# Optimization experiments

Measured on AMD Instinct MI355X. Metric: run time of the kernel, lower is better.

The kernel has to match this reference:

```python
import jax, jax.numpy as jnp
import numpy as np

N_NODES = 50000
N_EDGES = 1_600_000
IN_DIM = 128
HID = 64


def gcn_conv(x, src, dst, w, W, b, n):
    # PyG GCNConv(normalize=True, add_self_loops=True):
    # add self loops with weight 1, sym-normalize, x@W (no bias in lin), scatter-add, +bias
    loop = jnp.arange(n)
    s = jnp.concatenate([src, loop])
    d = jnp.concatenate([dst, loop])
    ww = jnp.concatenate([w, jnp.ones((n,), w.dtype)])
    deg = jax.ops.segment_sum(ww, d, num_segments=n)                 # [n]
    dis = jnp.where(deg > 0, jax.lax.rsqrt(deg), 0.0)                # deg^{-1/2}, inf->0
    norm = dis[s] * ww * dis[d]                                      # [E+n]
    h = x @ W                                                        # [n, out]
    msg = h[s] * norm[:, None]                                       # gather + scale
    out = jax.ops.segment_sum(msg, d, num_segments=n)                # scatter-add at dst
    return out + b


def setup_inputs() -> dict:
    key = jax.random.key(0)
    ks = jax.random.split(key, 9)
    X = jax.random.normal(ks[0], (N_NODES, IN_DIM), dtype=jnp.float32)
    edge_index = jax.random.randint(ks[1], (2, N_EDGES), 0, N_NODES, dtype=jnp.int64)
    edge_weight = jax.random.uniform(ks[2], (N_EDGES,), dtype=jnp.float32)
    s1 = 1.0 / np.sqrt(IN_DIM)
    s2 = 1.0 / np.sqrt(HID)
    W1 = jax.random.uniform(ks[3], (IN_DIM, HID), jnp.float32, -s1, s1)
    b1 = jax.random.uniform(ks[4], (HID,), jnp.float32, -s1, s1)
    W2 = jax.random.uniform(ks[5], (HID, HID), jnp.float32, -s2, s2)
    b2 = jax.random.uniform(ks[6], (HID,), jnp.float32, -s2, s2)
    Wl = jax.random.uniform(ks[7], (HID, 1), jnp.float32, -s2, s2)
    bl = jax.random.uniform(ks[8], (1,), jnp.float32, -s2, s2)
    return {"X": X, "edge_index": edge_index, "edge_weight": edge_weight,
            "W1": W1, "b1": b1, "W2": W2, "b2": b2, "Wl": Wl, "bl": bl}


def reference(X, edge_index, edge_weight, W1, b1, W2, b2, Wl, bl):
    n = X.shape[0]
    src, dst = edge_index[0], edge_index[1]
    h = jax.nn.relu(gcn_conv(X, src, dst, edge_weight, W1, b1, n))
    # F.dropout(p=0.2) is identity in eval mode
    h = jax.nn.relu(gcn_conv(h, src, dst, edge_weight, W2, b2, n))
    return jax.nn.sigmoid(h @ Wl + bl).squeeze(1)   # [n]
```

## Files before the change

### kernel.cpp

```cpp
#include <hip/hip_runtime.h>

typedef float f32x2 __attribute__((ext_vector_type(2)));

#define A2B 512
#define A2T 512
#define STG 3200

__device__ __forceinline__ long ld_idx(const void* idx, long pos, int is64) {
  return is64 ? (long)((const long long*)idx)[pos]
              : (long)((const int*)idx)[pos];
}

__device__ __forceinline__ int detect_is64(const void* idx) {
  const unsigned long long* p = (const unsigned long long*)idx;
  unsigned long long v = p[threadIdx.x & 63];
  return (__ballot((v >> 32) != 0ull) == 0ull) ? 1 : 0;
}

__device__ __forceinline__ int swz_group(int bid, int GP) {
  int r = bid & 7, q = bid >> 3;
  int j = q / GP;
  int i = q - j * GP;
  return (r + 8 * j) * GP + i;
}

__device__ __forceinline__ uint4 pack16_fp8(const float* acc) {
  uint4 o;
  unsigned v;
  v = 0;
  v = __builtin_amdgcn_cvt_pk_fp8_f32(acc[0],  acc[1],  v, false);
  v = __builtin_amdgcn_cvt_pk_fp8_f32(acc[2],  acc[3],  v, true);
  o.x = v; v = 0;
  v = __builtin_amdgcn_cvt_pk_fp8_f32(acc[4],  acc[5],  v, false);
  v = __builtin_amdgcn_cvt_pk_fp8_f32(acc[6],  acc[7],  v, true);
  o.y = v; v = 0;
  v = __builtin_amdgcn_cvt_pk_fp8_f32(acc[8],  acc[9],  v, false);
  v = __builtin_amdgcn_cvt_pk_fp8_f32(acc[10], acc[11], v, true);
  o.z = v; v = 0;
  v = __builtin_amdgcn_cvt_pk_fp8_f32(acc[12], acc[13], v, false);
  v = __builtin_amdgcn_cvt_pk_fp8_f32(acc[14], acc[15], v, true);
  o.w = v;
  return o;
}

__global__ __launch_bounds__(256) void k_front(const void* __restrict__ idx,
                                               unsigned* __restrict__ histT,
                                               long E, int chunk, unsigned M) {
  __shared__ unsigned cnt[256];
  const int t = threadIdx.x;
  const int b = blockIdx.x;
  const int is64 = detect_is64(idx);
  cnt[t] = 0;
  __syncthreads();
  const long e0 = (long)b * chunk;
  long e1 = e0 + chunk; if (e1 > E) e1 = E;
  for (long e = e0 + t; e < e1; e += 256) {
    unsigned d = (unsigned)ld_idx(idx, E + e, is64);
    atomicAdd(&cnt[__umulhi(d, M)], 1u);
  }
  __syncthreads();
  histT[(size_t)t * A2B + b] = cnt[t];
}

__global__ __launch_bounds__(256) void k_colscan(const unsigned* __restrict__ histT,
                                                 unsigned* __restrict__ baseT,
                                                 unsigned* __restrict__ colsum) {
  __shared__ unsigned sh[256];
  const int k = blockIdx.x, t = threadIdx.x;
  const uint2 v = ((const uint2*)(histT + (size_t)k * A2B))[t];
  unsigned s = v.x + v.y;
  sh[t] = s;
  __syncthreads();
  for (int off = 1; off < 256; off <<= 1) {
    unsigned u = (t >= off) ? sh[t - off] : 0;
    __syncthreads();
    sh[t] += u;
    __syncthreads();
  }
  unsigned excl = sh[t] - s;
  uint2 o; o.x = excl; o.y = excl + v.x;
  ((uint2*)(baseT + (size_t)k * A2B))[t] = o;
  if (t == 255) colsum[k] = sh[255];
}

__global__ __launch_bounds__(A2T) void k_bucket(const void* __restrict__ idx,
                                                const float* __restrict__ w,
                                                const unsigned* __restrict__ baseT,
                                                const unsigned* __restrict__ colsum,
                                                uint2* __restrict__ recs,
                                                long E, int chunk, unsigned M,
                                                const float* __restrict__ X,
                                                const float* __restrict__ W1,
                                                unsigned char* __restrict__ h, int n) {
  __shared__ uint2 stage[4096];
  __shared__ unsigned cnt[256], lofs[256], lbase[256], bcol[256], scanb[256];
  const int t = threadIdx.x;
  if (blockIdx.x >= A2B) {
    float* Ws = (float*)stage;
    for (int i = t; i < 2048; i += A2T)
      ((float4*)Ws)[i] = ((const float4*)W1)[i];
    __syncthreads();
    int gid = (blockIdx.x - A2B) * A2T + t;
    int node = gid >> 2;
    int fg = (gid & 3) * 16;
    if (node >= n) return;
    const float4* xr4 = (const float4*)(X + (size_t)node * 128);
    float acc[16];
#pragma unroll
    for (int f = 0; f < 16; ++f) acc[f] = 0.0f;
    for (int k4 = 0; k4 < 32; ++k4) {
      float4 x = xr4[k4];
#pragma unroll
      for (int kk = 0; kk < 4; ++kk) {
        float xv = (kk == 0) ? x.x : (kk == 1) ? x.y : (kk == 2) ? x.z : x.w;
        const float4* wrow = (const float4*)(Ws + (k4 * 4 + kk) * 64 + fg);
#pragma unroll
        for (int f4 = 0; f4 < 4; ++f4) {
          float4 wv = wrow[f4];
          acc[f4 * 4 + 0] = fmaf(xv, wv.x, acc[f4 * 4 + 0]);
          acc[f4 * 4 + 1] = fmaf(xv, wv.y, acc[f4 * 4 + 1]);
          acc[f4 * 4 + 2] = fmaf(xv, wv.z, acc[f4 * 4 + 2]);
          acc[f4 * 4 + 3] = fmaf(xv, wv.w, acc[f4 * 4 + 3]);
        }
      }
    }
    *(uint4*)(h + (size_t)node * 64 + fg) = pack16_fp8(acc);
    return;
  }
  const int b = blockIdx.x;
  const long e0 = (long)b * chunk;
  long e1 = e0 + chunk; if (e1 > E) e1 = E;
  const int m = (int)(e1 - e0);
  const int is64 = detect_is64(idx);
  if (t < 256) scanb[t] = colsum[t];
  __syncthreads();
  for (int off = 1; off < 256; off <<= 1) {
    unsigned u = 0;
    if (t < 256 && t >= off) u = scanb[t - off];
    __syncthreads();
    if (t < 256) scanb[t] += u;
    __syncthreads();
  }
  if (t < 256) {
    bcol[t] = (scanb[t] - colsum[t]) + baseT[(size_t)t * A2B + b];
    cnt[t] = 0;
  }
  __syncthreads();
  unsigned short dc[8]; unsigned char kc[8];
  int nk = 0;
  for (long e = e0 + t; e < e1; e += A2T, ++nk) {
    unsigned d = (unsigned)ld_idx(idx, E + e, is64);
    unsigned kb = __umulhi(d, M);
    dc[nk] = (unsigned short)d; kc[nk] = (unsigned char)kb;
    atomicAdd(&cnt[kb], 1u);
  }
  __syncthreads();
  if (t < 256) scanb[t] = cnt[t];
  __syncthreads();
  for (int off = 1; off < 256; off <<= 1) {
    unsigned u = 0;
    if (t < 256 && t >= off) u = scanb[t - off];
    __syncthreads();
    if (t < 256) scanb[t] += u;
    __syncthreads();
  }
  if (t < 256) { unsigned ex = scanb[t] - cnt[t]; lbase[t] = ex; lofs[t] = ex; }
  __syncthreads();
  nk = 0;
  for (long e = e0 + t; e < e1; e += A2T, ++nk) {
    unsigned s = (unsigned)ld_idx(idx, e, is64);
    float wv = w[e];
    unsigned kb = kc[nk];
    unsigned pos = atomicAdd(&lofs[kb], 1u);
    stage[pos] = make_uint2(s | ((unsigned)dc[nk] << 16), __float_as_uint(wv));
  }
  __syncthreads();
  for (int i = t; i < m; i += A2T) {
    uint2 r = stage[i];
    unsigned kb = __umulhi(r.x >> 16, M);
    recs[bcol[kb] + (unsigned)i - lbase[kb]] = r;
  }
}

__global__ __launch_bounds__(1024) void k_bp(const uint2* __restrict__ recs,
                                             const unsigned* __restrict__ colsum,
                                             int* __restrict__ rowptr,
                                             float* __restrict__ dis,
                                             float2* __restrict__ edges,
                                             int n, int dwidth, long E) {
  __shared__ float wsum[256];
  __shared__ unsigned cnt[256], lofs[256], scanb[256];
  __shared__ int shr0, shr1;
  const int k = blockIdx.x, t = threadIdx.x;
  const int d0 = k * dwidth;
  if (t < 256) scanb[t] = colsum[t];
  __syncthreads();
  for (int off = 1; off < 256; off <<= 1) {
    unsigned u = 0;
    if (t < 256 && t >= off) u = scanb[t - off];
    __syncthreads();
    if (t < 256) scanb[t] += u;
    __syncthreads();
  }
  if (t == k) { shr1 = (int)scanb[t]; shr0 = (int)(scanb[t] - colsum[t]); }
  if (t < 256) { wsum[t] = 0.0f; cnt[t] = 0; }
  __syncthreads();
  const int r0 = shr0, r1 = shr1;
  const int m = r1 - r0;
  for (int i = t; i < m; i += 1024) {
    uint2 r = recs[r0 + i];
    int dl = (int)(r.x >> 16) - d0;
    atomicAdd(&cnt[dl], 1u);
    atomicAdd(&wsum[dl], __uint_as_float(r.y));
  }
  __syncthreads();
  if (t < 256) scanb[t] = cnt[t];
  __syncthreads();
  for (int off = 1; off < 256; off <<= 1) {
    unsigned u = 0;
    if (t < 256 && t >= off) u = scanb[t - off];
    __syncthreads();
    if (t < 256) scanb[t] += u;
    __syncthreads();
  }
  if (t < 256) {
    unsigned ex = scanb[t] - cnt[t];
    lofs[t] = (unsigned)r0 + ex;
    int d = d0 + t;
    if (t < dwidth && d < n) {
      rowptr[d] = r0 + (int)ex;
      dis[d] = rsqrtf(1.0f + wsum[t]);
    }
  }
  if (k == gridDim.x - 1 && t == 0) rowptr[n] = (int)E;
  __syncthreads();
  for (int i = t; i < m; i += 1024) {
    uint2 r = recs[r0 + i];
    unsigned pos = atomicAdd(&lofs[(int)(r.x >> 16) - d0], 1u);
    edges[pos] = make_float2(__uint_as_float(r.x & 0xffffu), __uint_as_float(r.y));
  }
}

__device__ __forceinline__ void gather_acc(const unsigned char* __restrict__ h,
                                           const float* __restrict__ dis,
                                           const float2* __restrict__ edges,
                                           int beg, int end, int eg, int fl,
                                           float* acc) {
  f32x2 a0 = {0.0f, 0.0f}, a1 = {0.0f, 0.0f}, a2 = {0.0f, 0.0f}, a3 = {0.0f, 0.0f};
  const unsigned char* hf = h + fl * 8;
  for (int base = beg; base < end; base += 48) {
    float2 rv[12];
#pragma unroll
    for (int s = 0; s < 12; ++s) {
      int idx = base + s * 4 + eg;
      rv[s] = edges[min(idx, end - 1)];
    }
    int sj[12];
    float nj[12];
#pragma unroll
    for (int s = 0; s < 12; ++s) {
      sj[s] = __float_as_int(rv[s].x);
      nj[s] = rv[s].y * dis[sj[s]];
    }
    uint2 hv[12];
#pragma unroll
    for (int s = 0; s < 12; ++s)
      hv[s] = *(const uint2*)(hf + (size_t)sj[s] * 64);
#pragma unroll
    for (int s = 0; s < 12; ++s) {
      float w = (base + s * 4 + eg < end) ? nj[s] : 0.0f;
      f32x2 nj2 = {w, w};
      a0 += __builtin_amdgcn_cvt_pk_f32_fp8(hv[s].x, false) * nj2;
      a1 += __builtin_amdgcn_cvt_pk_f32_fp8(hv[s].x, true)  * nj2;
      a2 += __builtin_amdgcn_cvt_pk_f32_fp8(hv[s].y, false) * nj2;
      a3 += __builtin_amdgcn_cvt_pk_f32_fp8(hv[s].y, true)  * nj2;
    }
  }
  acc[0] = a0[0]; acc[1] = a0[1]; acc[2] = a1[0]; acc[3] = a1[1];
  acc[4] = a2[0]; acc[5] = a2[1]; acc[6] = a3[0]; acc[7] = a3[1];
#pragma unroll
  for (int off = 8; off < 32; off <<= 1)
#pragma unroll
    for (int i = 0; i < 8; ++i) acc[i] += __shfl_xor(acc[i], off);
}

__device__ __forceinline__ void add_bias_self(const unsigned char* __restrict__ h,
                                              const float* __restrict__ b,
                                              int node, int fl, float s0, float* acc) {
  uint2 hv = *(const uint2*)(h + (size_t)node * 64 + fl * 8);
  f32x2 q0 = __builtin_amdgcn_cvt_pk_f32_fp8(hv.x, false);
  f32x2 q1 = __builtin_amdgcn_cvt_pk_f32_fp8(hv.x, true);
  f32x2 q2 = __builtin_amdgcn_cvt_pk_f32_fp8(hv.y, false);
  f32x2 q3 = __builtin_amdgcn_cvt_pk_f32_fp8(hv.y, true);
  float hs[8] = {q0[0], q0[1], q1[0], q1[1], q2[0], q2[1], q3[0], q3[1]};
  float4 bv0 = *(const float4*)(b + fl * 8);
  float4 bv1 = *(const float4*)(b + fl * 8 + 4);
  float bb[8] = {bv0.x, bv0.y, bv0.z, bv0.w, bv1.x, bv1.y, bv1.z, bv1.w};
  float s2 = s0 * s0;
#pragma unroll
  for (int i = 0; i < 8; ++i) acc[i] += bb[i] + hs[i] * s2;
}

__global__ __launch_bounds__(256) void k_gather_mid(const unsigned char* __restrict__ h,
                                                    const float* __restrict__ dis,
                                                    const float2* __restrict__ edges,
                                                    const int* __restrict__ rowptr,
                                                    const float* __restrict__ b1,
                                                    const float* __restrict__ W2,
                                                    unsigned char* __restrict__ h2,
                                                    int n, int GP) {
  __shared__ float W2s[64 * 64];
  __shared__ float xs[8 * 64];
  const int t = threadIdx.x;
  for (int i = t; i < 1024; i += 256)
    ((float4*)W2s)[i] = ((const float4*)W2)[i];
  int lane = t & 63;
  int l32 = lane & 31;
  int fl = lane & 7;
  int eg = (lane >> 3) & 3;
  int nl = t >> 5;
  const int g = swz_group(blockIdx.x, GP);
  int node = g * 8 + nl;
  int beg = 0, end = 0; float s0 = 0.0f;
  if (node < n) { beg = rowptr[node]; end = rowptr[node + 1]; s0 = dis[node]; }
  float acc[8];
  gather_acc(h, dis, edges, beg, end, eg, fl, acc);
  if (node < n) {
#pragma unroll
    for (int i = 0; i < 8; ++i) acc[i] *= s0;
    add_bias_self(h, b1, node, fl, s0, acc);
    if (eg == 0) {
#pragma unroll
      for (int i = 0; i < 8; ++i) xs[nl * 64 + fl * 8 + i] = fmaxf(acc[i], 0.0f);
    }
  }
  __syncthreads();
  int tl = l32;
  int node2 = g * 8 + (t >> 5);
  if (node2 >= n) return;
  const float* xrow = xs + (t >> 5) * 64;
  int f = tl * 2;
  float a0 = 0.0f, a1 = 0.0f;
#pragma unroll 8
  for (int k = 0; k < 64; ++k) {
    float xk = xrow[k];
    f32x2 wv = *(const f32x2*)(W2s + k * 64 + f);
    a0 = fmaf(xk, wv[0], a0);
    a1 = fmaf(xk, wv[1], a1);
  }
  unsigned v = __builtin_amdgcn_cvt_pk_fp8_f32(a0, a1, 0u, false);
  *(unsigned short*)(h2 + (size_t)node2 * 64 + f) = (unsigned short)v;
}

__global__ __launch_bounds__(256) void k_gather_fin(const unsigned char* __restrict__ h,
                                                    const float* __restrict__ dis,
                                                    const float2* __restrict__ edges,
                                                    const int* __restrict__ rowptr,
                                                    const float* __restrict__ b2,
                                                    const float* __restrict__ Wl,
                                                    const float* __restrict__ bl,
                                                    float* __restrict__ out,
                                                    int n, int GP) {
  int lane = threadIdx.x & 63;
  int l32 = lane & 31;
  int fl = lane & 7;
  int eg = (lane >> 3) & 3;
  const int g = swz_group(blockIdx.x, GP);
  int node = g * 8 + (int)(threadIdx.x >> 5);
  if (node >= n) return;
  int beg = rowptr[node], end = rowptr[node + 1];
  float s0 = dis[node];
  float acc[8];
  gather_acc(h, dis, edges, beg, end, eg, fl, acc);
#pragma unroll
  for (int i = 0; i < 8; ++i) acc[i] *= s0;
  add_bias_self(h, b2, node, fl, s0, acc);
  float4 wl0 = *(const float4*)(Wl + fl * 8);
  float4 wl1 = *(const float4*)(Wl + fl * 8 + 4);
  float wl[8] = {wl0.x, wl0.y, wl0.z, wl0.w, wl1.x, wl1.y, wl1.z, wl1.w};
  float v = 0.0f;
#pragma unroll
  for (int i = 0; i < 8; ++i) v += fmaxf(acc[i], 0.0f) * wl[i];
#pragma unroll
  for (int off = 1; off < 8; off <<= 1) v += __shfl_xor(v, off);
  if (l32 == 0) out[node] = 1.0f / (1.0f + expf(-(v + bl[0])));
}

extern "C" void kernel_launch(void* const* d_in, const int* in_sizes, int n_in,
                              void* d_out, int out_size, void* d_ws, size_t ws_size,
                              hipStream_t stream) {
  const float* X  = (const float*)d_in[0];
  const void*  EI = d_in[1];
  const float* EW = (const float*)d_in[2];
  const float* W1 = (const float*)d_in[3];
  const float* b1 = (const float*)d_in[4];
  const float* W2 = (const float*)d_in[5];
  const float* b2 = (const float*)d_in[6];
  const float* Wl = (const float*)d_in[7];
  const float* bl = (const float*)d_in[8];
  float* out = (float*)d_out;

  const int  n = in_sizes[0] / 128;
  const long E = (long)in_sizes[1] / 2;

  const int chunk  = (int)((E + A2B - 1) / A2B);
  const int dwidth = (((n + 255) / 256) + 7) & ~7;
  const int GP     = dwidth >> 3;
  const unsigned M = (unsigned)((0x100000000ULL + (unsigned)dwidth - 1) / (unsigned)dwidth);

  auto align = [](size_t x) { return (x + 255) & ~(size_t)255; };
  char* ws = (char*)d_ws;
  size_t off = 0;
  float*         dis    = (float*)(ws + off);         off += align((size_t)n * 4);
  int*           rowptr = (int*)(ws + off);           off += align((size_t)(n + 1) * 4);
  unsigned*      colsum = (unsigned*)(ws + off);      off += align(256 * 4);
  unsigned*      histT  = (unsigned*)(ws + off);      off += align((size_t)A2B * 256 * 4);
  unsigned*      baseT  = (unsigned*)(ws + off);      off += align((size_t)A2B * 256 * 4);
  uint2*         recs   = (uint2*)(ws + off);         off += align((size_t)E * 8);
  float2*        edges  = (float2*)(ws + off);        off += align((size_t)E * 8);
  unsigned char* A      = (unsigned char*)(ws + off); off += align((size_t)n * 64);
  unsigned char* A2     = (unsigned char*)(ws + off); off += align((size_t)n * 64);

  const int nbW  = 32 * dwidth;
  const int nbG  = (n * 4 + A2T - 1) / A2T;

  k_front<<<A2B, dim3(256), 0, stream>>>(EI, histT, E, chunk, M);
  k_colscan<<<256, 256, 0, stream>>>(histT, baseT, colsum);
  k_bucket<<<A2B + nbG, dim3(A2T), 0, stream>>>(EI, EW, baseT, colsum, recs, E, chunk, M,
                                                X, W1, A, n);
  k_bp<<<256, dim3(1024), 0, stream>>>(recs, colsum, rowptr, dis, edges, n, dwidth, E);

  k_gather_mid<<<nbW, dim3(256), 0, stream>>>(A, dis, edges, rowptr, b1, W2, A2, n, GP);
  k_gather_fin<<<nbW, dim3(256), 0, stream>>>(A2, dis, edges, rowptr, b2, Wl, bl, out, n, GP);
}
```

Before: 209.6 us.

## Use wave-shuffle scans and double bucketing block count

Replaces the shared-memory Hillis-Steele scans, which needed two barriers per step, with a wave-level shuffle scan plus a small cross-wave fixup, cutting barrier count in the colscan, bucket and bp kernels. The bucketing grid doubles from 512 to 1024 blocks, so each block handles half as many edges, the per-thread register arrays shrink to 4 entries, and colscan now reads four histogram entries per thread. The intent is more parallelism and less barrier overhead in the CSR build, at the cost of a larger transposed histogram and more blocks to schedule.

```diff
diff --git a/kernel.cpp b/kernel.cpp
--- a/kernel.cpp
+++ b/kernel.cpp
@@ -2,7 +2,7 @@
 
 typedef float f32x2 __attribute__((ext_vector_type(2)));
 
-#define A2B 512
+#define A2B 1024
 #define A2T 512
 #define STG 3200
 
@@ -22,6 +22,28 @@
   int j = q / GP;
   int i = q - j * GP;
   return (r + 8 * j) * GP + i;
+}
+
+__device__ __forceinline__ void scan256(unsigned* sh, unsigned* wsums, int t) {
+  unsigned v = 0;
+  if (t < 256) {
+    v = sh[t];
+#pragma unroll
+    for (int off = 1; off < 64; off <<= 1) {
+      unsigned u = __shfl_up(v, off, 64);
+      if ((t & 63) >= off) v += u;
+    }
+    if ((t & 63) == 63) wsums[t >> 6] = v;
+  }
+  __syncthreads();
+  if (t < 256) {
+    unsigned add = 0;
+    int wid = t >> 6;
+#pragma unroll
+    for (int i = 0; i < 3; ++i) if (i < wid) add += wsums[i];
+    sh[t] = v + add;
+  }
+  __syncthreads();
 }
 
 __device__ __forceinline__ uint4 pack16_fp8(const float* acc) {
@@ -65,21 +87,20 @@
 __global__ __launch_bounds__(256) void k_colscan(const unsigned* __restrict__ histT,
                                                  unsigned* __restrict__ baseT,
                                                  unsigned* __restrict__ colsum) {
-  __shared__ unsigned sh[256];
+  __shared__ unsigned sh[256], wsums[4];
   const int k = blockIdx.x, t = threadIdx.x;
-  const uint2 v = ((const uint2*)(histT + (size_t)k * A2B))[t];
-  unsigned s = v.x + v.y;
+  const uint4 v = ((const uint4*)(histT + (size_t)k * A2B))[t];
+  unsigned s = v.x + v.y + v.z + v.w;
   sh[t] = s;
   __syncthreads();
-  for (int off = 1; off < 256; off <<= 1) {
-    unsigned u = (t >= off) ? sh[t - off] : 0;
-    __syncthreads();
-    sh[t] += u;
-    __syncthreads();
-  }
+  scan256(sh, wsums, t);
   unsigned excl = sh[t] - s;
-  uint2 o; o.x = excl; o.y = excl + v.x;
-  ((uint2*)(baseT + (size_t)k * A2B))[t] = o;
+  uint4 o;
+  o.x = excl;
+  o.y = excl + v.x;
+  o.z = o.y + v.y;
+  o.w = o.z + v.z;
+  ((uint4*)(baseT + (size_t)k * A2B))[t] = o;
   if (t == 255) colsum[k] = sh[255];
 }
 
@@ -93,7 +114,7 @@
                                                 const float* __restrict__ W1,
                                                 unsigned char* __restrict__ h, int n) {
   __shared__ uint2 stage[4096];
-  __shared__ unsigned cnt[256], lofs[256], lbase[256], bcol[256], scanb[256];
+  __shared__ unsigned cnt[256], lofs[256], lbase[256], bcol[256], scanb[256], wsums[4];
   const int t = threadIdx.x;
   if (blockIdx.x >= A2B) {
     float* Ws = (float*)stage;
@@ -134,19 +155,13 @@
   const int is64 = detect_is64(idx);
   if (t < 256) scanb[t] = colsum[t];
   __syncthreads();
-  for (int off = 1; off < 256; off <<= 1) {
-    unsigned u = 0;
-    if (t < 256 && t >= off) u = scanb[t - off];
-    __syncthreads();
-    if (t < 256) scanb[t] += u;
-    __syncthreads();
-  }
+  scan256(scanb, wsums, t);
   if (t < 256) {
     bcol[t] = (scanb[t] - colsum[t]) + baseT[(size_t)t * A2B + b];
     cnt[t] = 0;
   }
   __syncthreads();
-  unsigned short dc[8]; unsigned char kc[8];
+  unsigned short dc[4]; unsigned char kc[4];
   int nk = 0;
   for (long e = e0 + t; e < e1; e += A2T, ++nk) {
     unsigned d = (unsigned)ld_idx(idx, E + e, is64);
@@ -157,13 +172,7 @@
   __syncthreads();
   if (t < 256) scanb[t] = cnt[t];
   __syncthreads();
-  for (int off = 1; off < 256; off <<= 1) {
-    unsigned u = 0;
-    if (t < 256 && t >= off) u = scanb[t - off];
-    __syncthreads();
-    if (t < 256) scanb[t] += u;
-    __syncthreads();
-  }
+  scan256(scanb, wsums, t);
   if (t < 256) { unsigned ex = scanb[t] - cnt[t]; lbase[t] = ex; lofs[t] = ex; }
   __syncthreads();
   nk = 0;
@@ -189,23 +198,16 @@
                                              float2* __restrict__ edges,
                                              int n, int dwidth, long E) {
   __shared__ float wsum[256];
-  __shared__ unsigned cnt[256], lofs[256], scanb[256];
-  __shared__ int shr0, shr1;
+  __shared__ unsigned cnt[256], lofs[256], scanb[256], wsums[4];
   const int k = blockIdx.x, t = threadIdx.x;
   const int d0 = k * dwidth;
   if (t < 256) scanb[t] = colsum[t];
   __syncthreads();
-  for (int off = 1; off < 256; off <<= 1) {
-    unsigned u = 0;
-    if (t < 256 && t >= off) u = scanb[t - off];
-    __syncthreads();
-    if (t < 256) scanb[t] += u;
-    __syncthreads();
-  }
-  if (t == k) { shr1 = (int)scanb[t]; shr0 = (int)(scanb[t] - colsum[t]); }
+  scan256(scanb, wsums, t);
+  const int r1 = (int)scanb[k];
+  const int r0 = r1 - (int)colsum[k];
   if (t < 256) { wsum[t] = 0.0f; cnt[t] = 0; }
   __syncthreads();
-  const int r0 = shr0, r1 = shr1;
   const int m = r1 - r0;
   for (int i = t; i < m; i += 1024) {
     uint2 r = recs[r0 + i];
@@ -216,13 +218,7 @@
   __syncthreads();
   if (t < 256) scanb[t] = cnt[t];
   __syncthreads();
-  for (int off = 1; off < 256; off <<= 1) {
-    unsigned u = 0;
-    if (t < 256 && t >= off) u = scanb[t - off];
-    __syncthreads();
-    if (t < 256) scanb[t] += u;
-    __syncthreads();
-  }
+  scan256(scanb, wsums, t);
   if (t < 256) {
     unsigned ex = scanb[t] - cnt[t];
     lofs[t] = (unsigned)r0 + ex;
```

After: 214.8 us. 1.02x slower.
